# Kernel optimization log

Hardware: AMD Instinct MI355X
Metric: run time of the kernel (lower is better)

The kernel has to match this reference:

```python
import jax, jax.numpy as jnp
import numpy as np

B, S, E = 2, 8192, 128


def setup_inputs() -> dict:
    key = jax.random.key(0)
    ks = jax.random.split(key, 7)
    sc = 1.0 / np.sqrt(E)
    return {
        "x": jax.random.normal(ks[0], (B, S, E), dtype=jnp.float32),
        "Wq": jax.random.normal(ks[1], (E, E), dtype=jnp.float32) * sc,
        "bq": jax.random.normal(ks[2], (E,), dtype=jnp.float32) * 0.01,
        "Wk": jax.random.normal(ks[3], (E, E), dtype=jnp.float32) * sc,
        "bk": jax.random.normal(ks[4], (E,), dtype=jnp.float32) * 0.01,
        "Wv": jax.random.normal(ks[5], (E, E), dtype=jnp.float32) * sc,
        "bv": jax.random.normal(ks[6], (E,), dtype=jnp.float32) * 0.01,
    }


def reference(x, Wq, bq, Wk, bk, Wv, bv):
    # x: [B, S, E]. Conv1d(k=1) == per-slice linear: out[b,s,o] = sum_e W[o,e] x[b,s,e] + b[o]
    embed_dim = x.shape[-1]
    Q = jnp.einsum("bse,oe->bso", x, Wq) + bq  # [B, S, E]
    K = jnp.einsum("bse,oe->bso", x, Wk) + bk
    V = jnp.einsum("bse,oe->bso", x, Wv) + bv
    scores = jnp.einsum("bsd,btd->bst", Q, K) / jnp.sqrt(
        jnp.asarray(embed_dim, dtype=x.dtype)
    )  # [B, S, S]
    A = jax.nn.softmax(scores, axis=-1)
    # torch: out = bmm(V^T_as[B,E,S], A^T)[.transpose] == sum_t A[b,s,t] V[b,t,e]
    out = jnp.einsum("bst,bte->bse", A, V)  # [B, S, E]
    return out
```

## Files before the change

### kernel.cpp

```cpp
#include <hip/hip_runtime.h>
#include <math.h>

#define NB 2
#define NS 8192
#define NE 128
#define NROWS (NB * NS)

typedef __attribute__((ext_vector_type(8))) short s8v;
typedef __attribute__((ext_vector_type(16))) float fx16;
typedef __attribute__((ext_vector_type(2))) unsigned int u2v;
typedef __attribute__((address_space(1))) const unsigned char as1c;
typedef __attribute__((address_space(3))) unsigned char as3t;

static __device__ __forceinline__ unsigned int pkbf(float a, float b) {
    unsigned int ua = __float_as_uint(a), ub = __float_as_uint(b);
    ua += 0x7FFFu + ((ua >> 16) & 1u);
    ub += 0x7FFFu + ((ub >> 16) & 1u);
    return (ua >> 16) | (ub & 0xFFFF0000u);
}

static __device__ __forceinline__ unsigned int cvtpk(float a, float b) {
    unsigned int r;
    asm("v_cvt_pk_bf16_f32 %0, %1, %2" : "=v"(r) : "v"(a), "v"(b));
    return r;
}

__global__ __launch_bounds__(256, 2)
void qkv_kernel(const float* __restrict__ x,
                const float* __restrict__ Wq, const float* __restrict__ bq,
                const float* __restrict__ Wk, const float* __restrict__ bk,
                const float* __restrict__ Wv, const float* __restrict__ bv,
                unsigned short* __restrict__ qkv)
{
    __shared__ unsigned short WhL[64 * 136];
    __shared__ unsigned short WlL[64 * 136];

    const int t    = threadIdx.x;
    const int rblk = blockIdx.x * 128;
    const int mat  = blockIdx.y;
    const int o0   = blockIdx.z * 64;

    const float* W    = (mat == 0) ? Wq : (mat == 1) ? Wk : Wv;
    const float* bias = (mat == 0) ? bq : (mat == 1) ? bk : bv;
    unsigned short* out = qkv + (size_t)mat * NROWS * NE;
    const float osc = (mat == 0) ? 0.1275174460620886f : 1.0f;

    {
        const int r = t >> 2, cg = (t & 3) * 32;
        #pragma unroll
        for (int j = 0; j < 4; ++j) {
            const float* wp = &W[(size_t)(o0 + r) * NE + cg + j * 8];
            float4 a = *(const float4*)wp;
            float4 b = *(const float4*)(wp + 4);
            unsigned int h0 = pkbf(a.x, a.y), h1 = pkbf(a.z, a.w);
            unsigned int h2 = pkbf(b.x, b.y), h3 = pkbf(b.z, b.w);
            *(uint4*)&WhL[r * 136 + cg + j * 8] = make_uint4(h0, h1, h2, h3);
            float l0 = a.x - __uint_as_float(h0 << 16);
            float l1 = a.y - __uint_as_float(h0 & 0xFFFF0000u);
            float l2 = a.z - __uint_as_float(h1 << 16);
            float l3 = a.w - __uint_as_float(h1 & 0xFFFF0000u);
            float l4 = b.x - __uint_as_float(h2 << 16);
            float l5 = b.y - __uint_as_float(h2 & 0xFFFF0000u);
            float l6 = b.z - __uint_as_float(h3 << 16);
            float l7 = b.w - __uint_as_float(h3 & 0xFFFF0000u);
            *(uint4*)&WlL[r * 136 + cg + j * 8] =
                make_uint4(pkbf(l0, l1), pkbf(l2, l3), pkbf(l4, l5), pkbf(l6, l7));
        }
    }
    __syncthreads();

    const int w = t >> 6, lane = t & 63, lq = lane & 31, h = lane >> 5;
    const int rw = rblk + w * 32;

    s8v xhf[8], xlf[8];
    #pragma unroll
    for (int s = 0; s < 8; ++s) {
        const float* xp = &x[(size_t)(rw + lq) * NE + s * 16 + h * 8];
        float4 a = *(const float4*)xp;
        float4 b = *(const float4*)(xp + 4);
        unsigned int h0 = pkbf(a.x, a.y), h1 = pkbf(a.z, a.w);
        unsigned int h2 = pkbf(b.x, b.y), h3 = pkbf(b.z, b.w);
        float l0 = a.x - __uint_as_float(h0 << 16);
        float l1 = a.y - __uint_as_float(h0 & 0xFFFF0000u);
        float l2 = a.z - __uint_as_float(h1 << 16);
        float l3 = a.w - __uint_as_float(h1 & 0xFFFF0000u);
        float l4 = b.x - __uint_as_float(h2 << 16);
        float l5 = b.y - __uint_as_float(h2 & 0xFFFF0000u);
        float l6 = b.z - __uint_as_float(h3 << 16);
        float l7 = b.w - __uint_as_float(h3 & 0xFFFF0000u);
        union { uint4 u; s8v v; } H, L;
        H.u = make_uint4(h0, h1, h2, h3);
        L.u = make_uint4(pkbf(l0, l1), pkbf(l2, l3), pkbf(l4, l5), pkbf(l6, l7));
        xhf[s] = H.v;
        xlf[s] = L.v;
    }

    fx16 acc[2];
    #pragma unroll
    for (int ot = 0; ot < 2; ++ot)
        #pragma unroll
        for (int i = 0; i < 16; ++i) acc[ot][i] = 0.f;

    #pragma unroll
    for (int s = 0; s < 8; ++s) {
        #pragma unroll
        for (int ot = 0; ot < 2; ++ot) {
            s8v wh = *(const s8v*)&WhL[(ot * 32 + lq) * 136 + s * 16 + h * 8];
            s8v wl = *(const s8v*)&WlL[(ot * 32 + lq) * 136 + s * 16 + h * 8];
            if (mat != 2) {
                acc[ot] = __builtin_amdgcn_mfma_f32_32x32x16_bf16(wh, xhf[s], acc[ot], 0, 0, 0);
                acc[ot] = __builtin_amdgcn_mfma_f32_32x32x16_bf16(wh, xlf[s], acc[ot], 0, 0, 0);
                acc[ot] = __builtin_amdgcn_mfma_f32_32x32x16_bf16(wl, xhf[s], acc[ot], 0, 0, 0);
            } else {
                acc[ot] = __builtin_amdgcn_mfma_f32_32x32x16_bf16(xhf[s], wh, acc[ot], 0, 0, 0);
                acc[ot] = __builtin_amdgcn_mfma_f32_32x32x16_bf16(xlf[s], wh, acc[ot], 0, 0, 0);
                acc[ot] = __builtin_amdgcn_mfma_f32_32x32x16_bf16(xhf[s], wl, acc[ot], 0, 0, 0);
            }
        }
    }

    if (mat != 2) {
        const size_t rbase = (size_t)(rw + lq) * NE;
        #pragma unroll
        for (int ot = 0; ot < 2; ++ot)
            #pragma unroll
            for (int g = 0; g < 4; ++g) {
                int ob = o0 + ot * 32 + 4 * h + 8 * g;
                float4 bb = *(const float4*)&bias[ob];
                float v0 = (acc[ot][4 * g + 0] + bb.x) * osc;
                float v1 = (acc[ot][4 * g + 1] + bb.y) * osc;
                float v2 = (acc[ot][4 * g + 2] + bb.z) * osc;
                float v3 = (acc[ot][4 * g + 3] + bb.w) * osc;
                *(uint2*)&out[rbase + ob] = make_uint2(pkbf(v0, v1), pkbf(v2, v3));
            }
    } else {
        const int bb_ = rw >> 13, kb = (rw & (NS - 1)) + 4 * h;
        #pragma unroll
        for (int ot = 0; ot < 2; ++ot) {
            int o = o0 + ot * 32 + lq;
            float bv = bias[o];
            size_t obase = ((size_t)(bb_ * NE + o) << 13) + kb;
            #pragma unroll
            for (int g = 0; g < 4; ++g) {
                float v0 = acc[ot][4 * g + 0] + bv;
                float v1 = acc[ot][4 * g + 1] + bv;
                float v2 = acc[ot][4 * g + 2] + bv;
                float v3 = acc[ot][4 * g + 3] + bv;
                *(uint2*)&out[obase + 8 * g] = make_uint2(pkbf(v0, v1), pkbf(v2, v3));
            }
        }
    }
}

__global__ __launch_bounds__(256, 1)
void attn_kernel(const unsigned short* __restrict__ qkv,
                 _Float16* __restrict__ pd,
                 _Float16* __restrict__ pw,
                 float* __restrict__ ml)
{
    __shared__ unsigned short kbuf[2][64 * 128];
    __shared__ unsigned short vbuf[2][64 * 128];

    const int t  = threadIdx.x;
    const int id = blockIdx.x;
    const int ks = id & 3;
    const int b  = (id >> 2) & 1;
    const int T  = id >> 3;

    const unsigned short* Qg = qkv;
    const unsigned short* Kg = qkv + (size_t)NROWS * NE;
    const unsigned short* Vb = qkv + (size_t)2 * NROWS * NE + ((size_t)b << 20);

    const int w = t >> 6, lane = t & 63, lq = lane & 31, h = lane >> 5;
    const int qbw = b * NS + T * 256 + w * 64;
    const size_t kvb = (size_t)b * NS * NE;
    const int kq0 = ks * 2048;

    s8v qfA[8], qfB[8];
    #pragma unroll
    for (int s = 0; s < 8; ++s) {
        qfA[s] = *(const s8v*)(Qg + (size_t)(qbw + lq) * NE + s * 16 + h * 8);
        qfB[s] = *(const s8v*)(Qg + (size_t)(qbw + 32 + lq) * NE + s * 16 + h * 8);
    }

    fx16 accA[4], accB[4];
    #pragma unroll
    for (int dt = 0; dt < 4; ++dt)
        #pragma unroll
        for (int i = 0; i < 16; ++i) { accA[dt][i] = 0.f; accB[dt][i] = 0.f; }

    float lA = 0.f, lB = 0.f;

    const unsigned short* gptr[8];
    if (w < 2) {
        #pragma unroll
        for (int j = 0; j < 8; ++j) {
            int i = 8 * w + j;
            int keyl = 4 * i + (lane >> 4);
            int c = (lane & 15) ^ (keyl & 7);
            gptr[j] = Kg + kvb + (size_t)(kq0 + keyl) * NE + c * 8;
        }
    } else {
        #pragma unroll
        for (int j = 0; j < 8; ++j) {
            int i = 8 * (w - 2) + j;
            int d = 8 * i + (lane >> 3);
            int g = (lane & 7) ^ (d & 7);
            gptr[j] = Vb + ((size_t)d << 13) + kq0 + g * 8;
        }
    }
    const int gstride = (w < 2) ? 64 * NE : 64;

    auto stage = [&](int bufi) {
        if (w < 2) {
            #pragma unroll
            for (int j = 0; j < 8; ++j) {
                __builtin_amdgcn_global_load_lds((as1c*)gptr[j],
                    (as3t*)&kbuf[bufi][(8 * w + j) * 512], 16, 0, 0);
                gptr[j] += gstride;
            }
        } else {
            #pragma unroll
            for (int j = 0; j < 8; ++j) {
                __builtin_amdgcn_global_load_lds((as1c*)gptr[j],
                    (as3t*)&vbuf[bufi][(8 * (w - 2) + j) * 512], 16, 0, 0);
                gptr[j] += gstride;
            }
        }
    };

    stage(0);
    __syncthreads();

#define PEXA(i) (stA[(i) >> 4][(i) & 15])
#define PEXB(i) (stB[(i) >> 4][(i) & 15])
    int buf = 0;
    const int swz = (lq & 7) * 8;

    for (int r = 0; r < 32; ++r) {
        if (r < 31) stage(buf ^ 1);

        fx16 stA[2], stB[2];
        #pragma unroll
        for (int mt = 0; mt < 2; ++mt)
            #pragma unroll
            for (int i = 0; i < 16; ++i) { stA[mt][i] = 0.f; stB[mt][i] = 0.f; }
        __builtin_amdgcn_s_setprio(1);
        #pragma unroll
        for (int s = 0; s < 8; ++s) {
            int co = ((s * 2 + h) * 8) ^ swz;
            s8v a0 = *(const s8v*)&kbuf[buf][lq * 128 + co];
            s8v a1 = *(const s8v*)&kbuf[buf][(32 + lq) * 128 + co];
            stA[0] = __builtin_amdgcn_mfma_f32_32x32x16_bf16(a0, qfA[s], stA[0], 0, 0, 0);
            stB[0] = __builtin_amdgcn_mfma_f32_32x32x16_bf16(a0, qfB[s], stB[0], 0, 0, 0);
            stA[1] = __builtin_amdgcn_mfma_f32_32x32x16_bf16(a1, qfA[s], stA[1], 0, 0, 0);
            stB[1] = __builtin_amdgcn_mfma_f32_32x32x16_bf16(a1, qfB[s], stB[1], 0, 0, 0);
        }
        __builtin_amdgcn_s_setprio(0);

        float aA0 = 0.f, aA1 = 0.f, aB0 = 0.f, aB1 = 0.f;
        #pragma unroll
        for (int i = 0; i < 32; i += 2) {
            PEXA(i)     = __builtin_amdgcn_exp2f(PEXA(i));
            PEXB(i)     = __builtin_amdgcn_exp2f(PEXB(i));
            PEXA(i + 1) = __builtin_amdgcn_exp2f(PEXA(i + 1));
            PEXB(i + 1) = __builtin_amdgcn_exp2f(PEXB(i + 1));
            aA0 += PEXA(i); aA1 += PEXA(i + 1);
            aB0 += PEXB(i); aB1 += PEXB(i + 1);
        }
        float lsA = aA0 + aA1, lsB = aB0 + aB1;
        lsA += __shfl_xor(lsA, 32);
        lsB += __shfl_xor(lsB, 32);
        lA += lsA;
        lB += lsB;

        #pragma unroll
        for (int s2 = 0; s2 < 4; ++s2) {
            unsigned int A0 = cvtpk(PEXA(s2 * 8 + 0), PEXA(s2 * 8 + 1));
            unsigned int A1 = cvtpk(PEXA(s2 * 8 + 2), PEXA(s2 * 8 + 3));
            unsigned int A2 = cvtpk(PEXA(s2 * 8 + 4), PEXA(s2 * 8 + 5));
            unsigned int A3 = cvtpk(PEXA(s2 * 8 + 6), PEXA(s2 * 8 + 7));
            u2v a02 = __builtin_amdgcn_permlane32_swap(A0, A2, false, false);
            u2v a13 = __builtin_amdgcn_permlane32_swap(A1, A3, false, false);
            unsigned int B0 = cvtpk(PEXB(s2 * 8 + 0), PEXB(s2 * 8 + 1));
            unsigned int B1 = cvtpk(PEXB(s2 * 8 + 2), PEXB(s2 * 8 + 3));
            unsigned int B2 = cvtpk(PEXB(s2 * 8 + 4), PEXB(s2 * 8 + 5));
            unsigned int B3 = cvtpk(PEXB(s2 * 8 + 6), PEXB(s2 * 8 + 7));
            u2v b02 = __builtin_amdgcn_permlane32_swap(B0, B2, false, false);
            u2v b13 = __builtin_amdgcn_permlane32_swap(B1, B3, false, false);
            union { unsigned int u[4]; s8v v; } pfA, pfB;
            pfA.u[0] = a02.x; pfA.u[1] = a13.x; pfA.u[2] = a02.y; pfA.u[3] = a13.y;
            pfB.u[0] = b02.x; pfB.u[1] = b13.x; pfB.u[2] = b02.y; pfB.u[3] = b13.y;
            int go = ((s2 * 2 + h) * 8) ^ swz;
            __builtin_amdgcn_s_setprio(1);
            #pragma unroll
            for (int dt = 0; dt < 4; ++dt) {
                s8v vf = *(const s8v*)&vbuf[buf][(lq + 32 * dt) * 64 + go];
                accA[dt] = __builtin_amdgcn_mfma_f32_32x32x16_bf16(pfA.v, vf, accA[dt], 0, 0, 0);
                accB[dt] = __builtin_amdgcn_mfma_f32_32x32x16_bf16(pfB.v, vf, accB[dt], 0, 0, 0);
            }
            __builtin_amdgcn_s_setprio(0);
        }

        __syncthreads();
        buf ^= 1;
    }
#undef PEXA
#undef PEXB

    if (lane < 32) {
        ml[(size_t)(qbw + lq) * 4 + ks]      = lA;
        ml[(size_t)(qbw + 32 + lq) * 4 + ks] = lB;
    }

    float invlA = 1.0f / lA, invlB = 1.0f / lB;
    _Float16* P = (ks < 2) ? pd : pw;
    const int slot = (ks & 1) * 128;
    #pragma unroll
    for (int rg = 0; rg < 16; ++rg) {
        int row = (rg & 3) + 8 * (rg >> 2) + 4 * h;
        float scA = __shfl(invlA, row);
        float scB = __shfl(invlB, row);
        size_t rbA = (size_t)(qbw + row) * 256 + slot;
        size_t rbB = (size_t)(qbw + 32 + row) * 256 + slot;
        #pragma unroll
        for (int dt = 0; dt < 4; ++dt) {
            P[rbA + lq + 32 * dt] = (_Float16)(accA[dt][rg] * scA);
            P[rbB + lq + 32 * dt] = (_Float16)(accB[dt][rg] * scB);
        }
    }
}

__global__ __launch_bounds__(256, 2)
void merge_kernel(const _Float16* __restrict__ pw,
                  const float* __restrict__ ml,
                  float* __restrict__ outp)
{
    const int gi = blockIdx.x * 256 + threadIdx.x;
    const int q = gi >> 4, d0 = (gi & 15) * 8;
    const _Float16* pd = (const _Float16*)outp;

    uint4 u0 = *(const uint4*)&pd[(size_t)q * 256 + d0];
    uint4 u1 = *(const uint4*)&pd[(size_t)q * 256 + 128 + d0];
    uint4 u2 = *(const uint4*)&pw[(size_t)q * 256 + d0];
    uint4 u3 = *(const uint4*)&pw[(size_t)q * 256 + 128 + d0];
    float l0 = ml[q * 4 + 0], l1 = ml[q * 4 + 1];
    float l2 = ml[q * 4 + 2], l3 = ml[q * 4 + 3];

    float inv = 1.f / (l0 + l1 + l2 + l3);
    float a0 = l0 * inv, a1 = l1 * inv, a2 = l2 * inv, a3 = l3 * inv;

    union { uint4 u; _Float16 hh[8]; } c0, c1, c2, c3;
    c0.u = u0; c1.u = u1; c2.u = u2; c3.u = u3;
    float ov[8];
    #pragma unroll
    for (int e = 0; e < 8; ++e)
        ov[e] = (float)c0.hh[e] * a0 + (float)c1.hh[e] * a1 +
                (float)c2.hh[e] * a2 + (float)c3.hh[e] * a3;

    *(float4*)&outp[(size_t)q * 128 + d0]     = *(float4*)&ov[0];
    *(float4*)&outp[(size_t)q * 128 + d0 + 4] = *(float4*)&ov[4];
}

extern "C" void kernel_launch(void* const* d_in, const int* in_sizes, int n_in,
                              void* d_out, int out_size, void* d_ws, size_t ws_size,
                              hipStream_t stream)
{
    const float* x  = (const float*)d_in[0];
    const float* Wq = (const float*)d_in[1];
    const float* bq = (const float*)d_in[2];
    const float* Wk = (const float*)d_in[3];
    const float* bk = (const float*)d_in[4];
    const float* Wv = (const float*)d_in[5];
    const float* bv = (const float*)d_in[6];
    float* out = (float*)d_out;

    unsigned char* ws = (unsigned char*)d_ws;
    unsigned short* qkv = (unsigned short*)ws;
    _Float16* pw = (_Float16*)(ws + (size_t)3 * NROWS * NE * 2);
    float* mlp = (float*)(ws + (size_t)3 * NROWS * NE * 2
                             + (size_t)NROWS * 256 * 2);

    dim3 g1(NROWS / 128, 3, 2);
    qkv_kernel<<<g1, 256, 0, stream>>>(x, Wq, bq, Wk, bk, Wv, bv, qkv);

    attn_kernel<<<256, 256, 0, stream>>>(qkv, (_Float16*)d_out, pw, mlp);
    merge_kernel<<<1024, 256, 0, stream>>>(pw, mlp, out);
}
```

Before: 170.3 us.

## Split attention keys eight ways and run two blocks per CU

```diff
diff --git a/kernel.cpp b/kernel.cpp
--- a/kernel.cpp
+++ b/kernel.cpp
@@ -113,8 +113,8 @@
                 acc[ot] = __builtin_amdgcn_mfma_f32_32x32x16_bf16(wl, xhf[s], acc[ot], 0, 0, 0);
             } else {
                 acc[ot] = __builtin_amdgcn_mfma_f32_32x32x16_bf16(xhf[s], wh, acc[ot], 0, 0, 0);
+                acc[ot] = __builtin_amdgcn_mfma_f32_32x32x16_bf16(xhf[s], wl, acc[ot], 0, 0, 0);
                 acc[ot] = __builtin_amdgcn_mfma_f32_32x32x16_bf16(xlf[s], wh, acc[ot], 0, 0, 0);
-                acc[ot] = __builtin_amdgcn_mfma_f32_32x32x16_bf16(xhf[s], wl, acc[ot], 0, 0, 0);
             }
         }
     }
@@ -152,7 +152,7 @@
     }
 }
 
-__global__ __launch_bounds__(256, 1)
+__global__ __launch_bounds__(256, 2)
 void attn_kernel(const unsigned short* __restrict__ qkv,
                  _Float16* __restrict__ pd,
                  _Float16* __restrict__ pw,
@@ -163,9 +163,9 @@
 
     const int t  = threadIdx.x;
     const int id = blockIdx.x;
-    const int ks = id & 3;
-    const int b  = (id >> 2) & 1;
-    const int T  = id >> 3;
+    const int ks = id & 7;
+    const int b  = (id >> 3) & 1;
+    const int T  = id >> 4;
 
     const unsigned short* Qg = qkv;
     const unsigned short* Kg = qkv + (size_t)NROWS * NE;
@@ -174,7 +174,7 @@
     const int w = t >> 6, lane = t & 63, lq = lane & 31, h = lane >> 5;
     const int qbw = b * NS + T * 256 + w * 64;
     const size_t kvb = (size_t)b * NS * NE;
-    const int kq0 = ks * 2048;
+    const int kq0 = ks * 1024;
 
     s8v qfA[8], qfB[8];
     #pragma unroll
@@ -237,8 +237,8 @@
     int buf = 0;
     const int swz = (lq & 7) * 8;
 
-    for (int r = 0; r < 32; ++r) {
-        if (r < 31) stage(buf ^ 1);
+    for (int r = 0; r < 16; ++r) {
+        if (r < 15) stage(buf ^ 1);
 
         fx16 stA[2], stB[2];
         #pragma unroll
@@ -309,20 +309,22 @@
 #undef PEXB
 
     if (lane < 32) {
-        ml[(size_t)(qbw + lq) * 4 + ks]      = lA;
-        ml[(size_t)(qbw + 32 + lq) * 4 + ks] = lB;
+        ml[(size_t)(qbw + lq) * 8 + ks]      = lA;
+        ml[(size_t)(qbw + 32 + lq) * 8 + ks] = lB;
     }
 
     float invlA = 1.0f / lA, invlB = 1.0f / lB;
-    _Float16* P = (ks < 2) ? pd : pw;
-    const int slot = (ks & 1) * 128;
+    _Float16* P;
+    int rstride, slot;
+    if (ks < 2) { P = pd; rstride = 256; slot = ks * 128; }
+    else        { P = pw; rstride = 768; slot = (ks - 2) * 128; }
     #pragma unroll
     for (int rg = 0; rg < 16; ++rg) {
         int row = (rg & 3) + 8 * (rg >> 2) + 4 * h;
         float scA = __shfl(invlA, row);
         float scB = __shfl(invlB, row);
-        size_t rbA = (size_t)(qbw + row) * 256 + slot;
-        size_t rbB = (size_t)(qbw + 32 + row) * 256 + slot;
+        size_t rbA = (size_t)(qbw + row) * rstride + slot;
+        size_t rbB = (size_t)(qbw + 32 + row) * rstride + slot;
         #pragma unroll
         for (int dt = 0; dt < 4; ++dt) {
             P[rbA + lq + 32 * dt] = (_Float16)(accA[dt][rg] * scA);
@@ -340,23 +342,28 @@
     const int q = gi >> 4, d0 = (gi & 15) * 8;
     const _Float16* pd = (const _Float16*)outp;
 
-    uint4 u0 = *(const uint4*)&pd[(size_t)q * 256 + d0];
-    uint4 u1 = *(const uint4*)&pd[(size_t)q * 256 + 128 + d0];
-    uint4 u2 = *(const uint4*)&pw[(size_t)q * 256 + d0];
-    uint4 u3 = *(const uint4*)&pw[(size_t)q * 256 + 128 + d0];
-    float l0 = ml[q * 4 + 0], l1 = ml[q * 4 + 1];
-    float l2 = ml[q * 4 + 2], l3 = ml[q * 4 + 3];
-
-    float inv = 1.f / (l0 + l1 + l2 + l3);
-    float a0 = l0 * inv, a1 = l1 * inv, a2 = l2 * inv, a3 = l3 * inv;
-
-    union { uint4 u; _Float16 hh[8]; } c0, c1, c2, c3;
-    c0.u = u0; c1.u = u1; c2.u = u2; c3.u = u3;
+    union { uint4 u; _Float16 hh[8]; } c[8];
+    c[0].u = *(const uint4*)&pd[(size_t)q * 256 + d0];
+    c[1].u = *(const uint4*)&pd[(size_t)q * 256 + 128 + d0];
+    #pragma unroll
+    for (int p = 0; p < 6; ++p)
+        c[2 + p].u = *(const uint4*)&pw[(size_t)q * 768 + p * 128 + d0];
+
+    float4 la = *(const float4*)&ml[q * 8];
+    float4 lb = *(const float4*)&ml[q * 8 + 4];
+    float inv = 1.f / ((la.x + la.y + la.z + la.w) + (lb.x + lb.y + lb.z + lb.w));
+    float wg[8] = { la.x * inv, la.y * inv, la.z * inv, la.w * inv,
+                    lb.x * inv, lb.y * inv, lb.z * inv, lb.w * inv };
+
     float ov[8];
     #pragma unroll
-    for (int e = 0; e < 8; ++e)
-        ov[e] = (float)c0.hh[e] * a0 + (float)c1.hh[e] * a1 +
-                (float)c2.hh[e] * a2 + (float)c3.hh[e] * a3;
+    for (int e = 0; e < 8; ++e) {
+        float s = 0.f;
+        #pragma unroll
+        for (int p = 0; p < 8; ++p)
+            s += (float)c[p].hh[e] * wg[p];
+        ov[e] = s;
+    }
 
     *(float4*)&outp[(size_t)q * 128 + d0]     = *(float4*)&ov[0];
     *(float4*)&outp[(size_t)q * 128 + d0 + 4] = *(float4*)&ov[4];
@@ -379,11 +386,11 @@
     unsigned short* qkv = (unsigned short*)ws;
     _Float16* pw = (_Float16*)(ws + (size_t)3 * NROWS * NE * 2);
     float* mlp = (float*)(ws + (size_t)3 * NROWS * NE * 2
-                             + (size_t)NROWS * 256 * 2);
+                             + (size_t)NROWS * 768 * 2);
 
     dim3 g1(NROWS / 128, 3, 2);
     qkv_kernel<<<g1, 256, 0, stream>>>(x, Wq, bq, Wk, bk, Wv, bv, qkv);
 
-    attn_kernel<<<256, 256, 0, stream>>>(qkv, (_Float16*)d_out, pw, mlp);
+    attn_kernel<<<512, 256, 0, stream>>>(qkv, (_Float16*)d_out, pw, mlp);
     merge_kernel<<<1024, 256, 0, stream>>>(pw, mlp, out);
 }
```

Result: slower. 192.4 us (+13.0%).
